# Kernel optimization log

Hardware: AMD Instinct MI355X
Metric: run time of the kernel (lower is better)

## Reference

```python
import jax, jax.numpy as jnp
import numpy as np
from jax import lax

CURRICULUM_EP = 12
LI, LS, LW = 0.5, 0.8, 3.0


def _gauss_win(ws, C, dtype):
    coords = jnp.arange(ws, dtype=jnp.float32) - ws // 2
    g = jnp.exp(-coords ** 2 / (2 * 1.5 ** 2))
    win = g[None, :] * g[:, None]
    win = win / win.sum()
    # depthwise kernel, OIHW with I=1, O=C
    return jnp.broadcast_to(win[None, None], (C, 1, ws, ws)).astype(dtype)


def _dwconv(x, win, p, C):
    return lax.conv_general_dilated(
        x, win, window_strides=(1, 1), padding=[(p, p), (p, p)],
        dimension_numbers=('NCHW', 'OIHW', 'NCHW'), feature_group_count=C)


def diff_ssim(x, y, ws=11):
    C1, C2 = 0.01 ** 2, 0.03 ** 2
    C = x.shape[1]
    p = ws // 2
    win = _gauss_win(ws, C, x.dtype)
    mx = _dwconv(x, win, p, C)
    my = _dwconv(y, win, p, C)
    sxx = _dwconv(x * x, win, p, C) - mx ** 2
    syy = _dwconv(y * y, win, p, C) - my ** 2
    sxy = _dwconv(x * y, win, p, C) - mx * my
    ssim_map = (2 * mx * my + C1) * (2 * sxy + C2) / ((mx ** 2 + my ** 2 + C1) * (sxx + syy + C2))
    return ssim_map.mean()


def setup_inputs() -> dict:
    key = jax.random.key(0)
    k1, k2, k3, k4 = jax.random.split(key, 4)
    B, C, H, W = 16, 3, 512, 512
    NB = 1024  # watermark bits
    eps = 1e-4
    cover = jax.random.uniform(k1, (B, C, H, W), dtype=jnp.float32)
    wmed = jax.random.uniform(k2, (B, C, H, W), dtype=jnp.float32)
    wm_orig = jax.random.uniform(k3, (B, NB), dtype=jnp.float32)
    wm_ext = jnp.clip(jax.random.uniform(k4, (B, NB), dtype=jnp.float32), eps, 1.0 - eps)
    return {"cover": cover, "wmed": wmed, "wm_orig": wm_orig, "wm_ext": wm_ext, "epoch": 20}


def reference(cover, wmed, wm_orig, wm_ext, epoch):
    ml = jnp.mean((wmed - cover) ** 2)
    sv = diff_ssim(wmed, cover)
    sl = 1.0 - sv
    wl = jnp.mean(-(wm_orig * jnp.log(wm_ext) + (1.0 - wm_orig) * jnp.log(1.0 - wm_ext)))
    if epoch <= CURRICULUM_EP:
        w_img, w_ssim = 0.05, 0.05
    else:
        progress = min(1.0, (epoch - CURRICULUM_EP) / 10.0)
        w_img = 0.05 + (LI - 0.05) * progress
        w_ssim = 0.05 + (LS - 0.05) * progress
    total = w_img * ml + w_ssim * sl + LW * wl
    return (total, ml, sv, wl)
```

## Files before the change

kernel.cpp:

```cpp
#include <hip/hip_runtime.h>
#include <math.h>

#define H_IMG 512
#define W_IMG 512
#define TW 32
#define CH 64
#define NCHUNK 4
#define STRIP (CH*NCHUNK)
#define HALO 5
#define WS11 11
#define RING 75
#define RS 36
#define FSTR (RING*RS)
#define NTHREADS 256

typedef float f2 __attribute__((ext_vector_type(2)));

__host__ __device__ constexpr float WT(int t) {
    return (t==0||t==10) ? 0.00102838f :
           (t==1||t==9)  ? 0.00759873f :
           (t==2||t==8)  ? 0.03600075f :
           (t==3||t==7)  ? 0.10936070f :
           (t==4||t==6)  ? 0.21300556f :
           (t==5)        ? 0.26601172f : 0.0f;
}

static __device__ __forceinline__ f2 splat2(float v) { f2 r = {v, v}; return r; }

__global__ __launch_bounds__(NTHREADS, 3) void ssim_mse_tile(
        const float* __restrict__ cover, const float* __restrict__ wmed,
        float* __restrict__ part, int nParts) {
    __shared__ __align__(16) float rbuf[5*FSTR];

    const int tid = threadIdx.x;
    const int bx  = blockIdx.x & 15;
    const int ys  = (blockIdx.x >> 4) & 1;
    const int pl  = blockIdx.x >> 5;
    const size_t pbase = (size_t)pl * (H_IMG*W_IMG);
    const float* xp = wmed + pbase;
    const float* yp = cover + pbase;
    const int Y0  = ys << 8;
    const int tx0 = bx*TW - HALO;
    const bool xin = (bx != 0) && (bx != 15);

    float ssim_acc = 0.f, mse_acc = 0.f;

    for (int k = 0; k < NCHUNK; ++k) {
        const int nrows = (k == 0) ? (CH + 2*HALO) : CH;
        const int hr0   = (k == 0) ? -HALO : (CH*k + HALO);
        const int ntask = nrows << 3;

        for (int t = tid; t < ntask; t += NTHREADS) {
            const int r  = t >> 3, c0 = (t & 7) << 2;
            const int hr = hr0 + r;
            const int gy = Y0 + hr;
            const int slot = (hr + HALO) % RING;
            const bool rok = (unsigned)gy < (unsigned)H_IMG;
            float xv[14], yv[14];
            if (rok && xin) {
                const int ga = tx0 + c0 - 3;
                const float* rx = xp + (size_t)gy*W_IMG + ga;
                const float* ry = yp + (size_t)gy*W_IMG + ga;
                float4 XA = *(const float4*)(rx);
                float4 XB = *(const float4*)(rx + 4);
                float4 XC = *(const float4*)(rx + 8);
                float4 XD = *(const float4*)(rx + 12);
                float  XE = rx[16];
                float4 YA = *(const float4*)(ry);
                float4 YB = *(const float4*)(ry + 4);
                float4 YC = *(const float4*)(ry + 8);
                float4 YD = *(const float4*)(ry + 12);
                float  YE = ry[16];
                xv[0]=XA.w;  xv[1]=XB.x;  xv[2]=XB.y;  xv[3]=XB.z;  xv[4]=XB.w;
                xv[5]=XC.x;  xv[6]=XC.y;  xv[7]=XC.z;  xv[8]=XC.w;  xv[9]=XD.x;
                xv[10]=XD.y; xv[11]=XD.z; xv[12]=XD.w; xv[13]=XE;
                yv[0]=YA.w;  yv[1]=YB.x;  yv[2]=YB.y;  yv[3]=YB.z;  yv[4]=YB.w;
                yv[5]=YC.x;  yv[6]=YC.y;  yv[7]=YC.z;  yv[8]=YC.w;  yv[9]=YD.x;
                yv[10]=YD.y; yv[11]=YD.z; yv[12]=YD.w; yv[13]=YE;
            } else if (rok) {
                const int gc = tx0 + c0;
                const float* prx = xp + (size_t)gy*W_IMG + gc;
                const float* pry = yp + (size_t)gy*W_IMG + gc;
#pragma unroll
                for (int j = 0; j < 14; ++j) {
                    bool ok = (unsigned)(gc + j) < (unsigned)W_IMG;
                    xv[j] = ok ? prx[j] : 0.f;
                    yv[j] = ok ? pry[j] : 0.f;
                }
            } else {
#pragma unroll
                for (int j = 0; j < 14; ++j) { xv[j] = 0.f; yv[j] = 0.f; }
            }

            if ((unsigned)hr < (unsigned)STRIP) {
#pragma unroll
                for (int j = 5; j < 9; ++j) {
                    float d = xv[j] - yv[j];
                    mse_acc = fmaf(d, d, mse_acc);
                }
            }

            f2 A[5][2];
#pragma unroll
            for (int f = 0; f < 5; ++f) { A[f][0] = splat2(0.f); A[f][1] = splat2(0.f); }
#pragma unroll
            for (int j = 0; j < 14; ++j) {
                float px = xv[j], py = yv[j];
                float pxx = px*px, pyy = py*py, pxy = px*py;
#pragma unroll
                for (int p = 0; p < 2; ++p) {
                    const int t0 = j - 2*p;
                    if (t0 >= 0 && t0 <= WS11) {
                        const f2 wp = {WT(t0), WT(t0-1)};
                        A[0][p] = __builtin_elementwise_fma(wp, splat2(px),  A[0][p]);
                        A[1][p] = __builtin_elementwise_fma(wp, splat2(py),  A[1][p]);
                        A[2][p] = __builtin_elementwise_fma(wp, splat2(pxx), A[2][p]);
                        A[3][p] = __builtin_elementwise_fma(wp, splat2(pyy), A[3][p]);
                        A[4][p] = __builtin_elementwise_fma(wp, splat2(pxy), A[4][p]);
                    }
                }
            }
            float* wb = &rbuf[slot*RS + c0];
#pragma unroll
            for (int f = 0; f < 5; ++f) {
                *(float4*)(wb + f*FSTR) =
                    make_float4(A[f][0].x, A[f][0].y, A[f][1].x, A[f][1].y);
            }
        }
        __syncthreads();

        {
            const int cb = (tid & 15) << 1;
            const int g  = tid >> 4;
            int sb = (CH*k + (g << 2)) % RING;
            f2 acc[5][4];
#pragma unroll
            for (int f = 0; f < 5; ++f)
#pragma unroll
                for (int o = 0; o < 4; ++o) acc[f][o] = splat2(0.f);
            const float* bp = rbuf + cb;
#pragma unroll
            for (int i = 0; i < 14; ++i) {
                int sl = sb + i; if (sl >= RING) sl -= RING;
                const float* rp = bp + sl*RS;
#pragma unroll
                for (int f = 0; f < 5; ++f) {
                    f2 v = *(const f2*)(rp + f*FSTR);
#pragma unroll
                    for (int o = 0; o < 4; ++o) {
                        const int tp = i - o;
                        if (tp >= 0 && tp <= 10)
                            acc[f][o] = __builtin_elementwise_fma(splat2(WT(tp)), v, acc[f][o]);
                    }
                }
            }
            const f2 c1v = {1e-4f, 1e-4f};
            const f2 c2v = {9e-4f, 9e-4f};
            const f2 two = {2.f, 2.f};
#pragma unroll
            for (int o = 0; o < 4; ++o) {
                f2 mx = acc[0][o], my = acc[1][o];
                f2 sxx = acc[2][o] - mx*mx;
                f2 syy = acc[3][o] - my*my;
                f2 sxy = acc[4][o] - mx*my;
                f2 num = (two*mx*my + c1v) * (two*sxy + c2v);
                f2 den = (mx*mx + my*my + c1v) * (sxx + syy + c2v);
                ssim_acc += __fdividef(num.x, den.x) + __fdividef(num.y, den.y);
            }
        }
        __syncthreads();
    }

#pragma unroll
    for (int off = 32; off > 0; off >>= 1) {
        ssim_acc += __shfl_down(ssim_acc, off);
        mse_acc  += __shfl_down(mse_acc, off);
    }
    const int wid = tid >> 6, lane = tid & 63;
    if (lane == 0) { rbuf[wid] = ssim_acc; rbuf[4+wid] = mse_acc; }
    __syncthreads();
    if (tid == 0) {
        part[blockIdx.x] = rbuf[0]+rbuf[1]+rbuf[2]+rbuf[3];
        part[nParts + blockIdx.x] = rbuf[4]+rbuf[5]+rbuf[6]+rbuf[7];
    }
}

#define FT 1024
__global__ __launch_bounds__(FT) void finalize_k(
        const float* __restrict__ part, int nParts,
        const float* __restrict__ wm_orig, const float* __restrict__ wm_ext,
        int nWm, const int* __restrict__ epoch_p,
        float* __restrict__ out, double inv_npix, double inv_nwm) {
    __shared__ double red[48];
    int tid = threadIdx.x;
    double s_ssim = 0.0, s_mse = 0.0, s_wl = 0.0;
    const float4* s4 = (const float4*)part;
    const float4* m4 = (const float4*)(part + nParts);
    int n4 = nParts >> 2;
    for (int i = tid; i < n4; i += FT) {
        float4 v = s4[i];
        s_ssim += (double)((v.x + v.y) + (v.z + v.w));
        float4 u = m4[i];
        s_mse  += (double)((u.x + u.y) + (u.z + u.w));
    }
    const float4* p4 = (const float4*)wm_orig;
    const float4* q4 = (const float4*)wm_ext;
    int w4 = nWm >> 2;
    for (int i = tid; i < w4; i += FT) {
        float4 p = p4[i], q = q4[i];
        float a;
        a  = -(p.x*__logf(q.x) + (1.f-p.x)*__logf(1.f-q.x));
        a += -(p.y*__logf(q.y) + (1.f-p.y)*__logf(1.f-q.y));
        a += -(p.z*__logf(q.z) + (1.f-p.z)*__logf(1.f-q.z));
        a += -(p.w*__logf(q.w) + (1.f-p.w)*__logf(1.f-q.w));
        s_wl += (double)a;
    }
#pragma unroll
    for (int off = 32; off > 0; off >>= 1) {
        s_ssim += __shfl_down(s_ssim, off);
        s_mse  += __shfl_down(s_mse, off);
        s_wl   += __shfl_down(s_wl, off);
    }
    int wid = tid >> 6, lane = tid & 63;
    if (lane == 0) { red[wid] = s_ssim; red[16+wid] = s_mse; red[32+wid] = s_wl; }
    __syncthreads();
    if (tid == 0) {
        double ssim_sum = 0.0, mse_sum = 0.0, wl_sum = 0.0;
        for (int i = 0; i < 16; ++i) {
            ssim_sum += red[i]; mse_sum += red[16+i]; wl_sum += red[32+i];
        }
        float sv = (float)(ssim_sum * inv_npix);
        float ml = (float)(mse_sum  * inv_npix);
        float wl = (float)(wl_sum   * inv_nwm);
        int e = *epoch_p;
        float w_img, w_ssim;
        if (e <= 12) {
            w_img = 0.05f; w_ssim = 0.05f;
        } else {
            float progress = fminf(1.0f, (float)(e - 12) / 10.0f);
            w_img  = 0.05f + (0.5f - 0.05f)*progress;
            w_ssim = 0.05f + (0.8f - 0.05f)*progress;
        }
        float sl = 1.0f - sv;
        float total = w_img*ml + w_ssim*sl + 3.0f*wl;
        out[0] = total;
        out[1] = ml;
        out[2] = sv;
        out[3] = wl;
    }
}

extern "C" void kernel_launch(void* const* d_in, const int* in_sizes, int n_in,
                              void* d_out, int out_size, void* d_ws, size_t ws_size,
                              hipStream_t stream) {
    const float* cover   = (const float*)d_in[0];
    const float* wmed    = (const float*)d_in[1];
    const float* wm_orig = (const float*)d_in[2];
    const float* wm_ext  = (const float*)d_in[3];
    const int*   epoch   = (const int*)d_in[4];
    float* out = (float*)d_out;

    int npix   = in_sizes[0];
    int planes = npix / (H_IMG * W_IMG);
    int nWm    = in_sizes[2];

    int nBlocks = 16 * 2 * planes;
    int nParts  = nBlocks;
    float* part = (float*)d_ws;

    ssim_mse_tile<<<nBlocks, NTHREADS, 0, stream>>>(cover, wmed, part, nParts);
    finalize_k<<<1, FT, 0, stream>>>(part, nParts, wm_orig, wm_ext, nWm,
                                     epoch, out,
                                     1.0 / (double)npix, 1.0 / (double)nWm);
}
```

Before: 190.4 us.

## Halve row chunk, split planes into four strips, remap vertical pass threads

Chunk height and the shared ring buffer shrink, and each image plane is split into four vertical strips instead of two, which doubles the grid. Launch bounds now ask for 5 blocks per CU. The vertical convolution pass is remapped so each thread handles one column and four rows, packing pairs of output rows into f2 FMAs with paired weights. The aim is to cut LDS and register use for higher occupancy and more parallelism, at the cost of recomputing more halo rows per strip.

```diff
diff --git a/kernel.cpp b/kernel.cpp
--- a/kernel.cpp
+++ b/kernel.cpp
@@ -4,12 +4,12 @@
 #define H_IMG 512
 #define W_IMG 512
 #define TW 32
-#define CH 64
+#define CH 32
 #define NCHUNK 4
 #define STRIP (CH*NCHUNK)
 #define HALO 5
 #define WS11 11
-#define RING 75
+#define RING 42
 #define RS 36
 #define FSTR (RING*RS)
 #define NTHREADS 256
@@ -27,19 +27,19 @@
 
 static __device__ __forceinline__ f2 splat2(float v) { f2 r = {v, v}; return r; }
 
-__global__ __launch_bounds__(NTHREADS, 3) void ssim_mse_tile(
+__global__ __launch_bounds__(NTHREADS, 5) void ssim_mse_tile(
         const float* __restrict__ cover, const float* __restrict__ wmed,
         float* __restrict__ part, int nParts) {
     __shared__ __align__(16) float rbuf[5*FSTR];
 
     const int tid = threadIdx.x;
     const int bx  = blockIdx.x & 15;
-    const int ys  = (blockIdx.x >> 4) & 1;
-    const int pl  = blockIdx.x >> 5;
+    const int ys  = (blockIdx.x >> 4) & 3;
+    const int pl  = blockIdx.x >> 6;
     const size_t pbase = (size_t)pl * (H_IMG*W_IMG);
     const float* xp = wmed + pbase;
     const float* yp = cover + pbase;
-    const int Y0  = ys << 8;
+    const int Y0  = ys << 7;
     const int tx0 = bx*TW - HALO;
     const bool xin = (bx != 0) && (bx != 15);
 
@@ -130,27 +130,29 @@
         __syncthreads();
 
         {
-            const int cb = (tid & 15) << 1;
-            const int g  = tid >> 4;
-            int sb = (CH*k + (g << 2)) % RING;
-            f2 acc[5][4];
-#pragma unroll
-            for (int f = 0; f < 5; ++f)
-#pragma unroll
-                for (int o = 0; o < 4; ++o) acc[f][o] = splat2(0.f);
-            const float* bp = rbuf + cb;
+            const int c  = tid & 31;
+            const int rg = tid >> 3 >> 2;
+            const int sb = (CH*k + (rg << 2)) % RING;
+            f2 acc[5][2];
+#pragma unroll
+            for (int f = 0; f < 5; ++f) {
+                acc[f][0] = splat2(0.f); acc[f][1] = splat2(0.f);
+            }
+            const float* bp = rbuf + c;
 #pragma unroll
             for (int i = 0; i < 14; ++i) {
                 int sl = sb + i; if (sl >= RING) sl -= RING;
                 const float* rp = bp + sl*RS;
 #pragma unroll
                 for (int f = 0; f < 5; ++f) {
-                    f2 v = *(const f2*)(rp + f*FSTR);
-#pragma unroll
-                    for (int o = 0; o < 4; ++o) {
-                        const int tp = i - o;
-                        if (tp >= 0 && tp <= 10)
-                            acc[f][o] = __builtin_elementwise_fma(splat2(WT(tp)), v, acc[f][o]);
+                    float v = rp[f*FSTR];
+#pragma unroll
+                    for (int p = 0; p < 2; ++p) {
+                        const int t0 = i - 2*p;
+                        if (t0 >= 0 && t0 <= WS11) {
+                            const f2 wp = {WT(t0), WT(t0-1)};
+                            acc[f][p] = __builtin_elementwise_fma(wp, splat2(v), acc[f][p]);
+                        }
                     }
                 }
             }
@@ -158,11 +160,11 @@
             const f2 c2v = {9e-4f, 9e-4f};
             const f2 two = {2.f, 2.f};
 #pragma unroll
-            for (int o = 0; o < 4; ++o) {
-                f2 mx = acc[0][o], my = acc[1][o];
-                f2 sxx = acc[2][o] - mx*mx;
-                f2 syy = acc[3][o] - my*my;
-                f2 sxy = acc[4][o] - mx*my;
+            for (int p = 0; p < 2; ++p) {
+                f2 mx = acc[0][p], my = acc[1][p];
+                f2 sxx = acc[2][p] - mx*mx;
+                f2 syy = acc[3][p] - my*my;
+                f2 sxy = acc[4][p] - mx*my;
                 f2 num = (two*mx*my + c1v) * (two*sxy + c2v);
                 f2 den = (mx*mx + my*my + c1v) * (sxx + syy + c2v);
                 ssim_acc += __fdividef(num.x, den.x) + __fdividef(num.y, den.y);
@@ -264,7 +266,7 @@
     int planes = npix / (H_IMG * W_IMG);
     int nWm    = in_sizes[2];
 
-    int nBlocks = 16 * 2 * planes;
+    int nBlocks = 16 * 4 * planes;
     int nParts  = nBlocks;
     float* part = (float*)d_ws;
 
```

After: 176.6 us. 7.2% less time.
